# Kernel optimization log

Measured on AMD Instinct MI355X. Metric: run time of the kernel, lower is better.

## Reference

```python
import jax, jax.numpy as jnp
import numpy as np

B, N, DIM, H, KVAL = 16, 1024, 128, 8, 4  # b divisible by K*K=16; mask batch = B//(K*K)=1


def setup_inputs() -> dict:
    key = jax.random.key(0)
    ks = jax.random.split(key, 6)
    x = jax.random.normal(ks[0], (B, N, DIM), jnp.float32)
    mask = (jax.random.uniform(ks[1], (B // (KVAL * KVAL), N - 1)) < 0.9).astype(jnp.float32)
    maps = (jax.random.uniform(ks[2], (B, N - 1)) < 0.9).astype(jnp.float32)
    Wqkv = jax.random.normal(ks[3], (DIM, 3 * DIM), jnp.float32) / np.sqrt(DIM)
    Wout = jax.random.normal(ks[4], (DIM, DIM), jnp.float32) / np.sqrt(DIM)
    bout = jnp.zeros((DIM,), jnp.float32)
    return {"x": x, "mask": mask, "maps": maps, "Wqkv": Wqkv, "Wout": Wout,
            "bout": bout, "K": KVAL}


def reference(x, mask, maps, Wqkv, Wout, bout, K):
    b, n, dim = x.shape
    h = H
    d = dim // h
    scale = dim ** -0.5
    qkv = x @ Wqkv                                  # [b, n, 3*dim]
    q, k, v = jnp.split(qkv, 3, axis=-1)

    def to_heads(t):
        return t.reshape(b, n, h, d).transpose(0, 2, 1, 3)  # [b, h, n, d]

    q, k, v = to_heads(q), to_heads(k), to_heads(v)
    dots = jnp.einsum('bhid,bhjd->bhij', q, k) * scale      # [b, h, n, n]
    mask_value = -jnp.finfo(dots.dtype).max

    # block mask: pad first key position with 1, broadcast over K*K batch block
    kk = K * K
    m = jnp.pad(mask, ((0, 0), (1, 0)), constant_values=1.0)  # [b//kk, n]
    dots = dots.reshape(b // kk, kk, h, n, n)
    m5 = m[:, None, None, None, :]
    dots = dots * m5 + mask_value * (1.0 - m5)
    dots = dots.reshape(b, h, n, n)

    # map mask: boolean fill per batch element
    mp = jnp.pad(maps, ((0, 0), (1, 0)), constant_values=1.0)  # [b, n]
    dots = jnp.where(mp[:, None, None, :] != 0, dots, mask_value)

    attn = jax.nn.softmax(dots, axis=-1)
    out = jnp.einsum('bhij,bhjd->bhid', attn, v)            # [b, h, n, d]
    out = out.transpose(0, 2, 1, 3).reshape(b, n, dim)      # [b, n, dim]
    return out @ Wout + bout
```

## Files before the change

### kernel.cpp

```cpp
#include <hip/hip_runtime.h>
#include <math.h>

#define B_   16
#define N_   1024
#define DIM_ 128
#define H_   8
#define D_   16
#define BH_  128

typedef unsigned short u16;
typedef unsigned int   u32;
typedef __attribute__((ext_vector_type(8))) short short8;
typedef __attribute__((ext_vector_type(4))) float f32x4;

__device__ __forceinline__ float bf2f(u16 u) {
    union { u32 i; float f; } c; c.i = ((u32)u) << 16; return c.f;
}
__device__ __forceinline__ u16 f2bf(float f) {
    union { float f; u32 i; } c; c.f = f;
    u32 r = c.i + 0x7FFFu + ((c.i >> 16) & 1u);
    return (u16)(r >> 16);
}
__device__ __forceinline__ u32 pack2bf(float a, float b) {
    union { float f; u32 i; } ca, cb; ca.f = a; cb.f = b;
    return ((ca.i + 0x8000u) >> 16) | ((cb.i + 0x8000u) & 0xFFFF0000u);
}
__device__ __forceinline__ u32 fbits(float f) {
    union { float f; u32 i; } c; c.f = f; return c.i;
}
__device__ __forceinline__ float fval(u32 i) {
    union { u32 i; float f; } c; c.i = i; return c.f;
}
__device__ __forceinline__ u32 pk_hi(float a, float b) {
    return (fbits(a) >> 16) | (fbits(b) & 0xFFFF0000u);
}
__device__ __forceinline__ float residf(float a) {
    return a - fval(fbits(a) & 0xFFFF0000u);
}
union frag8 { short8 s; u32 w[4]; };

#define BF_ONE  ((short)0x3F80)
#define BF_NINF ((u16)0xFF80)

#define SCALE_L2E (0.08838834764831845f * 1.4426950408889634f)

__global__ __launch_bounds__(256) void qkv_kernel(
    const float* __restrict__ x, const float* __restrict__ Wqkv,
    const float* __restrict__ maskp, const float* __restrict__ mapsp,
    u16* __restrict__ qws, u16* __restrict__ kws2, u16* __restrict__ vtws)
{
    const int tid  = threadIdx.x;
    const int wave = tid >> 6, lane = tid & 63;
    const int i16  = lane & 15, quad = lane >> 4;
    const int cb   = blockIdx.x % 6;
    const int rb   = blockIdx.x / 6;
    const int row_m = rb * 64 + wave * 16;

    const float* xp = x + (size_t)(row_m + i16) * 128;

    f32x4 acc0 = {0,0,0,0}, acc1 = {0,0,0,0}, acc2 = {0,0,0,0}, acc3 = {0,0,0,0};

    #pragma unroll
    for (int ks = 0; ks < 4; ks++) {
        const int k0 = ks * 32 + quad * 8;
        const float4 xa = *(const float4*)(xp + k0);
        const float4 xb = *(const float4*)(xp + k0 + 4);
        frag8 a_hi, a_lo;
        a_hi.w[0] = pk_hi(xa.x, xa.y); a_hi.w[1] = pk_hi(xa.z, xa.w);
        a_hi.w[2] = pk_hi(xb.x, xb.y); a_hi.w[3] = pk_hi(xb.z, xb.w);
        a_lo.w[0] = pk_hi(residf(xa.x), residf(xa.y));
        a_lo.w[1] = pk_hi(residf(xa.z), residf(xa.w));
        a_lo.w[2] = pk_hi(residf(xb.x), residf(xb.y));
        a_lo.w[3] = pk_hi(residf(xb.z), residf(xb.w));

        #define CT_STEP(CT, ACC) { \
            const float* wp = Wqkv + (size_t)k0 * 384 + (cb * 64 + CT * 16 + i16); \
            const float w0 = wp[0*384], w1 = wp[1*384], w2 = wp[2*384], w3 = wp[3*384]; \
            const float w4 = wp[4*384], w5 = wp[5*384], w6 = wp[6*384], w7 = wp[7*384]; \
            frag8 b_hi, b_lo; \
            b_hi.w[0] = pk_hi(w0, w1); b_hi.w[1] = pk_hi(w2, w3); \
            b_hi.w[2] = pk_hi(w4, w5); b_hi.w[3] = pk_hi(w6, w7); \
            b_lo.w[0] = pk_hi(residf(w0), residf(w1)); \
            b_lo.w[1] = pk_hi(residf(w2), residf(w3)); \
            b_lo.w[2] = pk_hi(residf(w4), residf(w5)); \
            b_lo.w[3] = pk_hi(residf(w6), residf(w7)); \
            ACC = __builtin_amdgcn_mfma_f32_16x16x32_bf16(a_hi.s, b_hi.s, ACC, 0, 0, 0); \
            ACC = __builtin_amdgcn_mfma_f32_16x16x32_bf16(a_lo.s, b_hi.s, ACC, 0, 0, 0); \
            ACC = __builtin_amdgcn_mfma_f32_16x16x32_bf16(a_hi.s, b_lo.s, ACC, 0, 0, 0); \
        }
        CT_STEP(0, acc0)
        CT_STEP(1, acc1)
        CT_STEP(2, acc2)
        CT_STEP(3, acc3)
        #undef CT_STEP
    }

    const int which = (cb * 64) >> 7;
    const int row   = row_m + quad * 4;
    const int bb    = row >> 10, n = row & 1023;

    #define STORE_CT(CT, ACC) { \
        const int c  = (cb * 64 + CT * 16) & 127; \
        const int h  = c >> 4; \
        const int bh = bb * 8 + h; \
        const int dd = i16; \
        if (which == 0) { \
            u16* p = qws + ((size_t)(bh * N_ + n)) * 16 + dd; \
            p[0]  = f2bf(ACC[0] * SCALE_L2E); p[16] = f2bf(ACC[1] * SCALE_L2E); \
            p[32] = f2bf(ACC[2] * SCALE_L2E); p[48] = f2bf(ACC[3] * SCALE_L2E); \
        } else if (which == 1) { \
            u16* p = kws2 + ((size_t)(bh * N_ + n)) * 32 + dd; \
            p[0]  = f2bf(ACC[0]); p[32] = f2bf(ACC[1]); \
            p[64] = f2bf(ACC[2]); p[96] = f2bf(ACC[3]); \
            if (dd == 0) { \
                _Pragma("unroll") \
                for (int r = 0; r < 4; r++) { \
                    const int nr = n + r; \
                    const bool valid = (nr == 0) || \
                        (maskp[nr - 1] != 0.0f && mapsp[bb * (N_ - 1) + nr - 1] != 0.0f); \
                    kws2[((size_t)(bh * N_ + nr)) * 32 + 16] = valid ? (u16)0 : BF_NINF; \
                } \
            } \
        } else { \
            *(ushort4*)(vtws + ((size_t)(bh * 16 + dd)) * N_ + n) = \
                make_ushort4(f2bf(ACC[0]), f2bf(ACC[1]), f2bf(ACC[2]), f2bf(ACC[3])); \
        } }
    STORE_CT(0, acc0)
    STORE_CT(1, acc1)
    STORE_CT(2, acc2)
    STORE_CT(3, acc3)
    #undef STORE_CT
}

__global__ __launch_bounds__(256) void attn_kernel(
    const u16* __restrict__ qws, const u16* __restrict__ kws2, const u16* __restrict__ vtws,
    u16* __restrict__ attn)
{
    const int tid  = threadIdx.x;
    const int wave = tid >> 6, lane = tid & 63;
    const int i16  = lane & 15, quad = lane >> 4;
    const int bh   = blockIdx.x;
    const int qb   = blockIdx.y;
    const int bb   = bh >> 3, h = bh & 7;
    const int qrow0 = qb * 256 + wave * 64;
    const int perm = ((i16 & 12) << 1) | (i16 & 3);

    const short8 zero8 = {0,0,0,0,0,0,0,0};
    const short8 ones8 = {BF_ONE,BF_ONE,BF_ONE,BF_ONE,BF_ONE,BF_ONE,BF_ONE,BF_ONE};

    short8 qf0 = zero8, qf1 = zero8, qf2 = zero8, qf3 = zero8;
    if (lane < 32) {
        const u16* qp = qws + ((size_t)(bh * N_ + qrow0 + i16)) * 16 + quad * 8;
        qf0 = *(const short8*)(qp);
        qf1 = *(const short8*)(qp + 256);
        qf2 = *(const short8*)(qp + 512);
        qf3 = *(const short8*)(qp + 768);
    } else if (lane < 48) {
        qf0[0] = BF_ONE; qf1[0] = BF_ONE; qf2[0] = BF_ONE; qf3[0] = BF_ONE;
    }

    const u16* kpA = kws2 + ((size_t)(bh * N_ + perm)) * 32 + quad * 8;
    const u16* kpB = kpA + 4 * 32;
    const u16* vp  = vtws + ((size_t)(bh * 16 + i16)) * N_ + quad * 8;

    f32x4 o0 = {0,0,0,0}, o1 = {0,0,0,0}, o2 = {0,0,0,0}, o3 = {0,0,0,0};
    f32x4 l0 = {0,0,0,0}, l1 = {0,0,0,0}, l2 = {0,0,0,0}, l3 = {0,0,0,0};
    const f32x4 zc = {0.f, 0.f, 0.f, 0.f};

    #pragma unroll 2
    for (int j0 = 0; j0 < N_; j0 += 32) {
        const short8 kfA = *(const short8*)kpA;
        const short8 kfB = *(const short8*)kpB;
        const short8 vf  = *(const short8*)vp;
        kpA += 32 * 32; kpB += 32 * 32; vp += 32;

        #define TILE(QF, O, L) { \
            f32x4 stA = __builtin_amdgcn_mfma_f32_16x16x32_bf16(kfA, QF, zc, 0, 0, 0); \
            f32x4 stB = __builtin_amdgcn_mfma_f32_16x16x32_bf16(kfB, QF, zc, 0, 0, 0); \
            float pA0 = __builtin_amdgcn_exp2f(stA[0]); \
            float pA1 = __builtin_amdgcn_exp2f(stA[1]); \
            float pA2 = __builtin_amdgcn_exp2f(stA[2]); \
            float pA3 = __builtin_amdgcn_exp2f(stA[3]); \
            float pB0 = __builtin_amdgcn_exp2f(stB[0]); \
            float pB1 = __builtin_amdgcn_exp2f(stB[1]); \
            float pB2 = __builtin_amdgcn_exp2f(stB[2]); \
            float pB3 = __builtin_amdgcn_exp2f(stB[3]); \
            frag8 pk; \
            pk.w[0] = pack2bf(pA0, pA1); pk.w[1] = pack2bf(pA2, pA3); \
            pk.w[2] = pack2bf(pB0, pB1); pk.w[3] = pack2bf(pB2, pB3); \
            O = __builtin_amdgcn_mfma_f32_16x16x32_bf16(vf,    pk.s, O, 0, 0, 0); \
            L = __builtin_amdgcn_mfma_f32_16x16x32_bf16(ones8, pk.s, L, 0, 0, 0); \
        }
        TILE(qf0, o0, l0)
        TILE(qf1, o1, l1)
        TILE(qf2, o2, l2)
        TILE(qf3, o3, l3)
        #undef TILE
    }

    #define OUT_T(T, O, L) { \
        const float inv = 1.0f / L[0]; \
        ushort4 pko = make_ushort4(f2bf(O[0] * inv), f2bf(O[1] * inv), \
                                   f2bf(O[2] * inv), f2bf(O[3] * inv)); \
        *(ushort4*)(attn + ((size_t)(bb * N_ + qrow0 + T * 16 + i16)) * DIM_ \
                    + h * 16 + quad * 4) = pko; }
    OUT_T(0, o0, l0)
    OUT_T(1, o1, l1)
    OUT_T(2, o2, l2)
    OUT_T(3, o3, l3)
    #undef OUT_T
}

struct bfpair { short hi, lo; };
__device__ __forceinline__ bfpair splitv(float v) {
    u16 h = f2bf(v);
    bfpair p;
    p.hi = (short)h;
    p.lo = (short)f2bf(v - bf2f(h));
    return p;
}
__global__ __launch_bounds__(256) void out_kernel(
    const u16* __restrict__ attnw, const float* __restrict__ Wout,
    const float* __restrict__ boutp, float* __restrict__ outp)
{
    const int tid  = threadIdx.x;
    const int wave = tid >> 6, lane = tid & 63;
    const int i16  = lane & 15, quad = lane >> 4;
    const int cb   = blockIdx.x & 1;
    const int rb   = blockIdx.x >> 1;
    const int row_m = rb * 64 + wave * 16;

    const u16* ap = attnw + (size_t)(row_m + i16) * 128;

    f32x4 acc0 = {0,0,0,0}, acc1 = {0,0,0,0}, acc2 = {0,0,0,0}, acc3 = {0,0,0,0};

    #pragma unroll
    for (int ks = 0; ks < 4; ks++) {
        const int k0 = ks * 32 + quad * 8;
        const short8 a = *(const short8*)(ap + k0);

        #define CT_STEP(CT, ACC) { \
            const float* wp = Wout + (size_t)k0 * 128 + (cb * 64 + CT * 16 + i16); \
            short8 b_hi, b_lo; \
            bfpair q; \
            q = splitv(wp[0*128]); b_hi[0] = q.hi; b_lo[0] = q.lo; \
            q = splitv(wp[1*128]); b_hi[1] = q.hi; b_lo[1] = q.lo; \
            q = splitv(wp[2*128]); b_hi[2] = q.hi; b_lo[2] = q.lo; \
            q = splitv(wp[3*128]); b_hi[3] = q.hi; b_lo[3] = q.lo; \
            q = splitv(wp[4*128]); b_hi[4] = q.hi; b_lo[4] = q.lo; \
            q = splitv(wp[5*128]); b_hi[5] = q.hi; b_lo[5] = q.lo; \
            q = splitv(wp[6*128]); b_hi[6] = q.hi; b_lo[6] = q.lo; \
            q = splitv(wp[7*128]); b_hi[7] = q.hi; b_lo[7] = q.lo; \
            ACC = __builtin_amdgcn_mfma_f32_16x16x32_bf16(a, b_hi, ACC, 0, 0, 0); \
            ACC = __builtin_amdgcn_mfma_f32_16x16x32_bf16(a, b_lo, ACC, 0, 0, 0); \
        }
        CT_STEP(0, acc0)
        CT_STEP(1, acc1)
        CT_STEP(2, acc2)
        CT_STEP(3, acc3)
        #undef CT_STEP
    }

    const int row = row_m + quad * 4;
    #define STORE_CT(CT, ACC) { \
        const int col = cb * 64 + CT * 16 + i16; \
        const float bo = boutp[col]; \
        float* op = outp + (size_t)row * 128 + col; \
        op[0 * 128] = ACC[0] + bo; \
        op[1 * 128] = ACC[1] + bo; \
        op[2 * 128] = ACC[2] + bo; \
        op[3 * 128] = ACC[3] + bo; \
    }
    STORE_CT(0, acc0)
    STORE_CT(1, acc1)
    STORE_CT(2, acc2)
    STORE_CT(3, acc3)
    #undef STORE_CT
}

extern "C" void kernel_launch(void* const* d_in, const int* in_sizes, int n_in,
                              void* d_out, int out_size, void* d_ws, size_t ws_size,
                              hipStream_t stream) {
    const float* x    = (const float*)d_in[0];
    const float* mask = (const float*)d_in[1];
    const float* maps = (const float*)d_in[2];
    const float* Wqkv = (const float*)d_in[3];
    const float* Wout = (const float*)d_in[4];
    const float* bout = (const float*)d_in[5];
    u16* qws  = (u16*)d_ws;
    u16* kws2 = qws  + (size_t)BH_ * N_ * 16;
    u16* vtws = kws2 + (size_t)BH_ * N_ * 32;
    u16* attn = vtws + (size_t)BH_ * N_ * 16;

    qkv_kernel<<<dim3(1536), dim3(256), 0, stream>>>(x, Wqkv, mask, maps, qws, kws2, vtws);
    attn_kernel<<<dim3(128, 4), dim3(256), 0, stream>>>(qws, kws2, vtws, attn);
    out_kernel<<<dim3(512), dim3(256), 0, stream>>>(attn, Wout, bout, (float*)d_out);
}
```

Measured before the change: 130.7 us.

## Pre-convert inputs and weights to bf16 and drop split-precision MFMA passes

Adds a prep kernel that converts x to bf16 and writes Wqkv and Wout as transposed bf16 arrays. The QKV and output projections then run a single bf16 MFMA per tile, replacing the hi/lo split passes (three MFMAs in QKV, two in the output projection) and their strided fp32 weight loads. This removes per-block conversion ALU work and the extra MFMAs but adds a kernel launch plus a pass over x. It also lowers projection accuracy to plain bf16.

New measurement: 134.9 us. 1.03x slower.

```diff
diff --git a/kernel.cpp b/kernel.cpp
--- a/kernel.cpp
+++ b/kernel.cpp
@@ -25,18 +25,6 @@
     union { float f; u32 i; } ca, cb; ca.f = a; cb.f = b;
     return ((ca.i + 0x8000u) >> 16) | ((cb.i + 0x8000u) & 0xFFFF0000u);
 }
-__device__ __forceinline__ u32 fbits(float f) {
-    union { float f; u32 i; } c; c.f = f; return c.i;
-}
-__device__ __forceinline__ float fval(u32 i) {
-    union { u32 i; float f; } c; c.i = i; return c.f;
-}
-__device__ __forceinline__ u32 pk_hi(float a, float b) {
-    return (fbits(a) >> 16) | (fbits(b) & 0xFFFF0000u);
-}
-__device__ __forceinline__ float residf(float a) {
-    return a - fval(fbits(a) & 0xFFFF0000u);
-}
 union frag8 { short8 s; u32 w[4]; };
 
 #define BF_ONE  ((short)0x3F80)
@@ -44,8 +32,32 @@
 
 #define SCALE_L2E (0.08838834764831845f * 1.4426950408889634f)
 
+__global__ __launch_bounds__(256) void prep_kernel(
+    const float* __restrict__ x, const float* __restrict__ Wqkv,
+    const float* __restrict__ Wout,
+    u16* __restrict__ xb, u16* __restrict__ wqkvb, u16* __restrict__ woutb)
+{
+    const int b = blockIdx.x, tid = threadIdx.x;
+    if (b < 2048) {
+        const int i = b * 256 + tid;
+        float4 v = ((const float4*)x)[i];
+        ushort4 o = make_ushort4(f2bf(v.x), f2bf(v.y), f2bf(v.z), f2bf(v.w));
+        *(ushort4*)(xb + (size_t)i * 4) = o;
+    } else {
+        const int t = (b - 2048) * 256 + tid;
+        if (t < 49152) {
+            const int k = t / 384, col = t - k * 384;
+            wqkvb[(size_t)col * 128 + k] = f2bf(Wqkv[t]);
+        } else {
+            const int t2 = t - 49152;
+            const int k = t2 >> 7, col = t2 & 127;
+            woutb[(size_t)col * 128 + k] = f2bf(Wout[t2]);
+        }
+    }
+}
+
 __global__ __launch_bounds__(256) void qkv_kernel(
-    const float* __restrict__ x, const float* __restrict__ Wqkv,
+    const u16* __restrict__ xb, const u16* __restrict__ wqkvb,
     const float* __restrict__ maskp, const float* __restrict__ mapsp,
     u16* __restrict__ qws, u16* __restrict__ kws2, u16* __restrict__ vtws)
 {
@@ -56,43 +68,23 @@
     const int rb   = blockIdx.x / 6;
     const int row_m = rb * 64 + wave * 16;
 
-    const float* xp = x + (size_t)(row_m + i16) * 128;
+    const u16* xp = xb + (size_t)(row_m + i16) * 128;
+    const u16* wb = wqkvb + (size_t)(cb * 64 + i16) * 128;
 
     f32x4 acc0 = {0,0,0,0}, acc1 = {0,0,0,0}, acc2 = {0,0,0,0}, acc3 = {0,0,0,0};
 
     #pragma unroll
     for (int ks = 0; ks < 4; ks++) {
         const int k0 = ks * 32 + quad * 8;
-        const float4 xa = *(const float4*)(xp + k0);
-        const float4 xb = *(const float4*)(xp + k0 + 4);
-        frag8 a_hi, a_lo;
-        a_hi.w[0] = pk_hi(xa.x, xa.y); a_hi.w[1] = pk_hi(xa.z, xa.w);
-        a_hi.w[2] = pk_hi(xb.x, xb.y); a_hi.w[3] = pk_hi(xb.z, xb.w);
-        a_lo.w[0] = pk_hi(residf(xa.x), residf(xa.y));
-        a_lo.w[1] = pk_hi(residf(xa.z), residf(xa.w));
-        a_lo.w[2] = pk_hi(residf(xb.x), residf(xb.y));
-        a_lo.w[3] = pk_hi(residf(xb.z), residf(xb.w));
-
-        #define CT_STEP(CT, ACC) { \
-            const float* wp = Wqkv + (size_t)k0 * 384 + (cb * 64 + CT * 16 + i16); \
-            const float w0 = wp[0*384], w1 = wp[1*384], w2 = wp[2*384], w3 = wp[3*384]; \
-            const float w4 = wp[4*384], w5 = wp[5*384], w6 = wp[6*384], w7 = wp[7*384]; \
-            frag8 b_hi, b_lo; \
-            b_hi.w[0] = pk_hi(w0, w1); b_hi.w[1] = pk_hi(w2, w3); \
-            b_hi.w[2] = pk_hi(w4, w5); b_hi.w[3] = pk_hi(w6, w7); \
-            b_lo.w[0] = pk_hi(residf(w0), residf(w1)); \
-            b_lo.w[1] = pk_hi(residf(w2), residf(w3)); \
-            b_lo.w[2] = pk_hi(residf(w4), residf(w5)); \
-            b_lo.w[3] = pk_hi(residf(w6), residf(w7)); \
-            ACC = __builtin_amdgcn_mfma_f32_16x16x32_bf16(a_hi.s, b_hi.s, ACC, 0, 0, 0); \
-            ACC = __builtin_amdgcn_mfma_f32_16x16x32_bf16(a_lo.s, b_hi.s, ACC, 0, 0, 0); \
-            ACC = __builtin_amdgcn_mfma_f32_16x16x32_bf16(a_hi.s, b_lo.s, ACC, 0, 0, 0); \
-        }
-        CT_STEP(0, acc0)
-        CT_STEP(1, acc1)
-        CT_STEP(2, acc2)
-        CT_STEP(3, acc3)
-        #undef CT_STEP
+        const short8 a = *(const short8*)(xp + k0);
+        acc0 = __builtin_amdgcn_mfma_f32_16x16x32_bf16(
+                   a, *(const short8*)(wb + k0), acc0, 0, 0, 0);
+        acc1 = __builtin_amdgcn_mfma_f32_16x16x32_bf16(
+                   a, *(const short8*)(wb + 16 * 128 + k0), acc1, 0, 0, 0);
+        acc2 = __builtin_amdgcn_mfma_f32_16x16x32_bf16(
+                   a, *(const short8*)(wb + 32 * 128 + k0), acc2, 0, 0, 0);
+        acc3 = __builtin_amdgcn_mfma_f32_16x16x32_bf16(
+                   a, *(const short8*)(wb + 48 * 128 + k0), acc3, 0, 0, 0);
     }
 
     const int which = (cb * 64) >> 7;
@@ -211,16 +203,8 @@
     #undef OUT_T
 }
 
-struct bfpair { short hi, lo; };
-__device__ __forceinline__ bfpair splitv(float v) {
-    u16 h = f2bf(v);
-    bfpair p;
-    p.hi = (short)h;
-    p.lo = (short)f2bf(v - bf2f(h));
-    return p;
-}
 __global__ __launch_bounds__(256) void out_kernel(
-    const u16* __restrict__ attnw, const float* __restrict__ Wout,
+    const u16* __restrict__ attnw, const u16* __restrict__ woutb,
     const float* __restrict__ boutp, float* __restrict__ outp)
 {
     const int tid  = threadIdx.x;
@@ -231,6 +215,7 @@
     const int row_m = rb * 64 + wave * 16;
 
     const u16* ap = attnw + (size_t)(row_m + i16) * 128;
+    const u16* wb = woutb + (size_t)(cb * 64 + i16) * 128;
 
     f32x4 acc0 = {0,0,0,0}, acc1 = {0,0,0,0}, acc2 = {0,0,0,0}, acc3 = {0,0,0,0};
 
@@ -238,27 +223,14 @@
     for (int ks = 0; ks < 4; ks++) {
         const int k0 = ks * 32 + quad * 8;
         const short8 a = *(const short8*)(ap + k0);
-
-        #define CT_STEP(CT, ACC) { \
-            const float* wp = Wout + (size_t)k0 * 128 + (cb * 64 + CT * 16 + i16); \
-            short8 b_hi, b_lo; \
-            bfpair q; \
-            q = splitv(wp[0*128]); b_hi[0] = q.hi; b_lo[0] = q.lo; \
-            q = splitv(wp[1*128]); b_hi[1] = q.hi; b_lo[1] = q.lo; \
-            q = splitv(wp[2*128]); b_hi[2] = q.hi; b_lo[2] = q.lo; \
-            q = splitv(wp[3*128]); b_hi[3] = q.hi; b_lo[3] = q.lo; \
-            q = splitv(wp[4*128]); b_hi[4] = q.hi; b_lo[4] = q.lo; \
-            q = splitv(wp[5*128]); b_hi[5] = q.hi; b_lo[5] = q.lo; \
-            q = splitv(wp[6*128]); b_hi[6] = q.hi; b_lo[6] = q.lo; \
-            q = splitv(wp[7*128]); b_hi[7] = q.hi; b_lo[7] = q.lo; \
-            ACC = __builtin_amdgcn_mfma_f32_16x16x32_bf16(a, b_hi, ACC, 0, 0, 0); \
-            ACC = __builtin_amdgcn_mfma_f32_16x16x32_bf16(a, b_lo, ACC, 0, 0, 0); \
-        }
-        CT_STEP(0, acc0)
-        CT_STEP(1, acc1)
-        CT_STEP(2, acc2)
-        CT_STEP(3, acc3)
-        #undef CT_STEP
+        acc0 = __builtin_amdgcn_mfma_f32_16x16x32_bf16(
+                   a, *(const short8*)(wb + k0), acc0, 0, 0, 0);
+        acc1 = __builtin_amdgcn_mfma_f32_16x16x32_bf16(
+                   a, *(const short8*)(wb + 16 * 128 + k0), acc1, 0, 0, 0);
+        acc2 = __builtin_amdgcn_mfma_f32_16x16x32_bf16(
+                   a, *(const short8*)(wb + 32 * 128 + k0), acc2, 0, 0, 0);
+        acc3 = __builtin_amdgcn_mfma_f32_16x16x32_bf16(
+                   a, *(const short8*)(wb + 48 * 128 + k0), acc3, 0, 0, 0);
     }
 
     const int row = row_m + quad * 4;
@@ -287,12 +259,16 @@
     const float* Wqkv = (const float*)d_in[3];
     const float* Wout = (const float*)d_in[4];
     const float* bout = (const float*)d_in[5];
-    u16* qws  = (u16*)d_ws;
-    u16* kws2 = qws  + (size_t)BH_ * N_ * 16;
-    u16* vtws = kws2 + (size_t)BH_ * N_ * 32;
-    u16* attn = vtws + (size_t)BH_ * N_ * 16;
-
-    qkv_kernel<<<dim3(1536), dim3(256), 0, stream>>>(x, Wqkv, mask, maps, qws, kws2, vtws);
+    u16* qws    = (u16*)d_ws;
+    u16* kws2   = qws   + (size_t)2 * 1024 * 1024;
+    u16* vtws   = kws2  + (size_t)4 * 1024 * 1024;
+    u16* attn   = vtws  + (size_t)2 * 1024 * 1024;
+    u16* xbws   = attn  + (size_t)2 * 1024 * 1024;
+    u16* wqkvb  = xbws  + (size_t)2 * 1024 * 1024;
+    u16* woutb  = wqkvb + (size_t)384 * 128;
+
+    prep_kernel<<<dim3(2304), dim3(256), 0, stream>>>(x, Wqkv, Wout, xbws, wqkvb, woutb);
+    qkv_kernel<<<dim3(1536), dim3(256), 0, stream>>>(xbws, wqkvb, mask, maps, qws, kws2, vtws);
     attn_kernel<<<dim3(128, 4), dim3(256), 0, stream>>>(qws, kws2, vtws, attn);
-    out_kernel<<<dim3(512), dim3(256), 0, stream>>>(attn, Wout, bout, (float*)d_out);
-}
+    out_kernel<<<dim3(512), dim3(256), 0, stream>>>(attn, woutb, bout, (float*)d_out);
+}
```
